# Kernel tuning notes

Hardware: AMD Instinct MI355X
Metric: run time of the kernel (lower is better)

Reference implementation:

```python
import jax, jax.numpy as jnp
import numpy as np

NUM_MODES = 192
LAYERS = [NUM_MODES * 2, 256, 128, 32]


def setup_inputs() -> dict:
    key = jax.random.key(0)
    ks = jax.random.split(key, 7)
    B, C, L = 64, 512, 1024
    x = jax.random.normal(ks[0], (B, C, L), dtype=jnp.float32)
    params = {}
    for i in range(3):
        fan_in, fan_out = LAYERS[i], LAYERS[i + 1]
        bound = 1.0 / np.sqrt(fan_in)
        params[f"W{i+1}"] = jax.random.uniform(ks[1 + 2 * i], (fan_in, fan_out), dtype=jnp.float32, minval=-bound, maxval=bound)
        params[f"b{i+1}"] = jax.random.uniform(ks[2 + 2 * i], (fan_out,), dtype=jnp.float32, minval=-bound, maxval=bound)
    return {"x": x, **params}


def reference(x, W1, b1, W2, b2, W3, b3):
    # rfft over last dim -> complex [B, C, L//2+1]
    f = jnp.fft.rfft(x, axis=-1)
    # view_as_real + slice first NUM_MODES bins -> [B, C, NUM_MODES, 2] (real, imag interleaved)
    f = f[..., :NUM_MODES]
    feat = jnp.stack([f.real, f.imag], axis=-1).reshape(*x.shape[:-1], NUM_MODES * 2)
    h = jax.nn.leaky_relu(feat @ W1 + b1, negative_slope=0.01)
    h = jax.nn.leaky_relu(h @ W2 + b2, negative_slope=0.01)
    return h @ W3 + b3
```

## Files before the change

### kernel.cpp

```cpp
#include <hip/hip_runtime.h>
#include <hip/hip_bf16.h>

typedef __attribute__((ext_vector_type(8))) short short8;
typedef __attribute__((ext_vector_type(4))) float f32x4;

__device__ __forceinline__ short8 load_af(const unsigned short* p) {
  union { uint2 u[2]; short8 v; } r;
  r.u[0] = *(const uint2*)(p);
  r.u[1] = *(const uint2*)(p + 16);
  return r.v;
}

__device__ __forceinline__ unsigned int pk_bf16(float a, float b) {
  __hip_bfloat162 h = __float22bfloat162_rn(make_float2(a, b));
  return *(unsigned int*)&h;
}
__device__ __forceinline__ unsigned short s_bf16(float a) {
  __hip_bfloat16 h = __float2bfloat16(a);
  return *(unsigned short*)&h;
}

__global__ __launch_bounds__(256) void prep_kernel(
    const float* __restrict__ W1, const float* __restrict__ W2,
    const float* __restrict__ W3,
    unsigned short* __restrict__ fL1, unsigned short* __restrict__ fL2,
    unsigned short* __restrict__ fL3) {
  const int w = blockIdx.x * 4 + (threadIdx.x >> 6);
  const int lane = threadIdx.x & 63;
  const int rlo = lane & 15;
  const int q4 = (lane >> 4) << 2;

  if (w < 512) {
    const int nt = w >> 5, kk = w & 31;
    const int col = nt * 16 + rlo;
    const int k0 = kk * 32 + q4;
    float pc[8], ps[8], dc[8], dsn[8], acc[8];
#pragma unroll
    for (int e = 0; e < 8; ++e) {
      int ke = k0 + (e & 3) + ((e >> 2) << 4);
      float ang = (float)ke * 6.135923151542565e-3f;
      float s, c;
      __sincosf(ang, &s, &c);
      dc[e] = c; dsn[e] = s;
      pc[e] = 1.f; ps[e] = 0.f;
      acc[e] = 0.f;
    }
    const float* pw = W1 + col;
#pragma unroll 2
    for (int m = 0; m < 192; ++m) {
      float wre = pw[0];
      float wio = pw[256];
      pw += 512;
#pragma unroll
      for (int e = 0; e < 8; ++e) {
        acc[e] = fmaf(pc[e], wre, acc[e]);
        acc[e] = fmaf(-ps[e], wio, acc[e]);
        float c2 = pc[e] * dc[e] - ps[e] * dsn[e];
        float s2 = ps[e] * dc[e] + pc[e] * dsn[e];
        pc[e] = c2; ps[e] = s2;
      }
    }
    uint4 v;
    v.x = pk_bf16(acc[0], acc[1]);
    v.y = pk_bf16(acc[2], acc[3]);
    v.z = pk_bf16(acc[4], acc[5]);
    v.w = pk_bf16(acc[6], acc[7]);
    *(uint4*)(fL1 + ((size_t)w * 64 + lane) * 8) = v;
  } else if (w < 576) {
    const int tl = w - 512;
    const int nt = tl >> 3, kk = tl & 7;
    const int col = nt * 16 + rlo;
    const int k0 = kk * 32 + q4;
    float a[8];
#pragma unroll
    for (int e = 0; e < 8; ++e) {
      int ke = k0 + (e & 3) + ((e >> 2) << 4);
      a[e] = W2[ke * 128 + col];
    }
    uint4 v;
    v.x = pk_bf16(a[0], a[1]); v.y = pk_bf16(a[2], a[3]);
    v.z = pk_bf16(a[4], a[5]); v.w = pk_bf16(a[6], a[7]);
    *(uint4*)(fL2 + ((size_t)tl * 64 + lane) * 8) = v;
  } else {
    const int tl = w - 576;
    const int nt = tl >> 2, kk = tl & 3;
    const int col = nt * 16 + rlo;
    const int k0 = kk * 32 + q4;
    float a[8];
#pragma unroll
    for (int e = 0; e < 8; ++e) {
      int ke = k0 + (e & 3) + ((e >> 2) << 4);
      a[e] = W3[ke * 32 + col];
    }
    uint4 v;
    v.x = pk_bf16(a[0], a[1]); v.y = pk_bf16(a[2], a[3]);
    v.z = pk_bf16(a[4], a[5]); v.w = pk_bf16(a[6], a[7]);
    *(uint4*)(fL3 + ((size_t)tl * 64 + lane) * 8) = v;
  }
}

#define XS_S 132
#define H1_S 260
#define H2_S 132

struct P2 {
  unsigned short h1[64 * H1_S];
  unsigned short h2[64 * H2_S];
};
union SH {
  unsigned short xs[2][64 * XS_S];
  P2 p2;
};

__global__ __launch_bounds__(256, 3) void mlp_kernel(
    const float* __restrict__ x,
    const float* __restrict__ b1, const float* __restrict__ b2,
    const float* __restrict__ b3,
    const unsigned short* __restrict__ fL1, const unsigned short* __restrict__ fL2,
    const unsigned short* __restrict__ fL3, float* __restrict__ out) {
  __shared__ SH sh;
  const int t = threadIdx.x;
  const int lane = t & 63;
  const int wid = t >> 6;
  const int rlo = lane & 15;
  const int g4 = (lane >> 4) << 2;
  const size_t row0 = (size_t)blockIdx.x * 64;
  const float* xb = x + row0 * 1024;

  f32x4 acc[4][4] = {};

  float4 st[8];
#pragma unroll
  for (int i = 0; i < 8; ++i) {
    int idx = i * 256 + t;
    int row = idx >> 5, cg = idx & 31;
    st[i] = *(const float4*)(xb + row * 1024 + cg * 4);
  }

  for (int kc = 0; kc < 8; ++kc) {
    unsigned short* xbuf = sh.xs[kc & 1];
#pragma unroll
    for (int i = 0; i < 8; ++i) {
      int idx = i * 256 + t;
      int row = idx >> 5, cg = idx & 31;
      uint2 wv;
      wv.x = pk_bf16(st[i].x, st[i].y);
      wv.y = pk_bf16(st[i].z, st[i].w);
      *(uint2*)(xbuf + row * XS_S + cg * 4) = wv;
    }
    if (kc < 7) {
#pragma unroll
      for (int i = 0; i < 8; ++i) {
        int idx = i * 256 + t;
        int row = idx >> 5, cg = idx & 31;
        st[i] = *(const float4*)(xb + row * 1024 + (kc + 1) * 128 + cg * 4);
      }
    }
    short8 bcur[4];
#pragma unroll
    for (int c = 0; c < 4; ++c)
      bcur[c] = *(const short8*)(fL1 +
                (((size_t)(wid * 4 + c) * 32 + kc * 4) * 64 + lane) * 8);
    __syncthreads();
#pragma unroll
    for (int ks = 0; ks < 4; ++ks) {
      short8 bnext[4];
      if (ks < 3) {
#pragma unroll
        for (int c = 0; c < 4; ++c)
          bnext[c] = *(const short8*)(fL1 +
                    (((size_t)(wid * 4 + c) * 32 + kc * 4 + ks + 1) * 64 + lane) * 8);
      }
      short8 af[4];
#pragma unroll
      for (int m = 0; m < 4; ++m)
        af[m] = load_af(xbuf + (m * 16 + rlo) * XS_S + ks * 32 + g4);
#pragma unroll
      for (int m = 0; m < 4; ++m)
#pragma unroll
        for (int c = 0; c < 4; ++c)
          acc[m][c] = __builtin_amdgcn_mfma_f32_16x16x32_bf16(af[m], bcur[c], acc[m][c], 0, 0, 0);
      if (ks < 3) {
#pragma unroll
        for (int c = 0; c < 4; ++c) bcur[c] = bnext[c];
      }
    }
  }
  __syncthreads();

  {
    float bv[4];
#pragma unroll
    for (int c = 0; c < 4; ++c) bv[c] = b1[wid * 64 + c * 16 + rlo];
#pragma unroll
    for (int m = 0; m < 4; ++m)
#pragma unroll
      for (int c = 0; c < 4; ++c)
#pragma unroll
        for (int r = 0; r < 4; ++r) {
          float v = acc[m][c][r] + bv[c];
          v = fmaxf(v, 0.01f * v);
          sh.p2.h1[(m * 16 + g4 + r) * H1_S + wid * 64 + c * 16 + rlo] = s_bf16(v);
        }
  }
  __syncthreads();

  f32x4 a2[4][2] = {};
#pragma unroll
  for (int ks = 0; ks < 8; ++ks) {
    short8 af[4];
#pragma unroll
    for (int m = 0; m < 4; ++m)
      af[m] = load_af(sh.p2.h1 + (m * 16 + rlo) * H1_S + ks * 32 + g4);
    short8 bfr[2];
#pragma unroll
    for (int c = 0; c < 2; ++c)
      bfr[c] = *(const short8*)(fL2 + (((size_t)(wid * 2 + c) * 8 + ks) * 64 + lane) * 8);
#pragma unroll
    for (int m = 0; m < 4; ++m)
#pragma unroll
      for (int c = 0; c < 2; ++c)
        a2[m][c] = __builtin_amdgcn_mfma_f32_16x16x32_bf16(af[m], bfr[c], a2[m][c], 0, 0, 0);
  }
  {
    float bv[2];
#pragma unroll
    for (int c = 0; c < 2; ++c) bv[c] = b2[wid * 32 + c * 16 + rlo];
#pragma unroll
    for (int m = 0; m < 4; ++m)
#pragma unroll
      for (int c = 0; c < 2; ++c)
#pragma unroll
        for (int r = 0; r < 4; ++r) {
          float v = a2[m][c][r] + bv[c];
          v = fmaxf(v, 0.01f * v);
          sh.p2.h2[(m * 16 + g4 + r) * H2_S + wid * 32 + c * 16 + rlo] = s_bf16(v);
        }
  }
  __syncthreads();

  f32x4 a3[2] = {};
#pragma unroll
  for (int ks = 0; ks < 4; ++ks) {
    short8 af = load_af(sh.p2.h2 + (wid * 16 + rlo) * H2_S + ks * 32 + g4);
#pragma unroll
    for (int c = 0; c < 2; ++c) {
      short8 bfr = *(const short8*)(fL3 + (((size_t)c * 4 + ks) * 64 + lane) * 8);
      a3[c] = __builtin_amdgcn_mfma_f32_16x16x32_bf16(af, bfr, a3[c], 0, 0, 0);
    }
  }
  {
    float bv[2];
    bv[0] = b3[rlo];
    bv[1] = b3[16 + rlo];
#pragma unroll
    for (int c = 0; c < 2; ++c)
#pragma unroll
      for (int r = 0; r < 4; ++r)
        out[(row0 + wid * 16 + g4 + r) * 32 + c * 16 + rlo] = a3[c][r] + bv[c];
  }
}

extern "C" void kernel_launch(void* const* d_in, const int* in_sizes, int n_in,
                              void* d_out, int out_size, void* d_ws, size_t ws_size,
                              hipStream_t stream) {
  const float* x  = (const float*)d_in[0];
  const float* W1 = (const float*)d_in[1];
  const float* b1 = (const float*)d_in[2];
  const float* W2 = (const float*)d_in[3];
  const float* b2 = (const float*)d_in[4];
  const float* W3 = (const float*)d_in[5];
  const float* b3 = (const float*)d_in[6];
  float* out = (float*)d_out;

  char* ws = (char*)d_ws;
  unsigned short* fL1 = (unsigned short*)ws;
  unsigned short* fL2 = (unsigned short*)(ws + 524288);
  unsigned short* fL3 = (unsigned short*)(ws + 589824);

  hipLaunchKernelGGL(prep_kernel, dim3(146), dim3(256), 0, stream,
                     W1, W2, W3, fL1, fL2, fL3);
  hipLaunchKernelGGL(mlp_kernel, dim3(512), dim3(256), 0, stream,
                     x, b1, b2, b3, fL1, fL2, fL3, out);
}
```

Baseline: 291.2 us.

## Load x fragments directly from global into registers, drop LDS staging

The first-layer GEMM no longer stages x tiles through a double-buffered LDS buffer. Each wave now loads its own MFMA A-fragments from global memory as float4 pairs, converts them to bf16 in registers, and prefetches one k-step ahead, which removes the LDS writes, reads and per-chunk barriers. The cost is that every one of the 4 waves reads the same x rows redundantly (4x global/L2 traffic for x), the loads are less coalesced, and register pressure rises, so launch bounds drop to 2 blocks per CU.

```diff
diff --git a/kernel.cpp b/kernel.cpp
--- a/kernel.cpp
+++ b/kernel.cpp
@@ -18,6 +18,15 @@
 __device__ __forceinline__ unsigned short s_bf16(float a) {
   __hip_bfloat16 h = __float2bfloat16(a);
   return *(unsigned short*)&h;
+}
+
+__device__ __forceinline__ short8 cvt_af(const float4& lo, const float4& hi) {
+  union { uint4 u; short8 v; } r;
+  r.u.x = pk_bf16(lo.x, lo.y);
+  r.u.y = pk_bf16(lo.z, lo.w);
+  r.u.z = pk_bf16(hi.x, hi.y);
+  r.u.w = pk_bf16(hi.z, hi.w);
+  return r.v;
 }
 
 __global__ __launch_bounds__(256) void prep_kernel(
@@ -99,94 +108,67 @@
   }
 }
 
-#define XS_S 132
 #define H1_S 260
 #define H2_S 132
 
-struct P2 {
-  unsigned short h1[64 * H1_S];
-  unsigned short h2[64 * H2_S];
-};
-union SH {
-  unsigned short xs[2][64 * XS_S];
-  P2 p2;
-};
-
-__global__ __launch_bounds__(256, 3) void mlp_kernel(
+__global__ __launch_bounds__(256, 2) void mlp_kernel(
     const float* __restrict__ x,
     const float* __restrict__ b1, const float* __restrict__ b2,
     const float* __restrict__ b3,
     const unsigned short* __restrict__ fL1, const unsigned short* __restrict__ fL2,
     const unsigned short* __restrict__ fL3, float* __restrict__ out) {
-  __shared__ SH sh;
+  __shared__ unsigned short h1s[64 * H1_S];
+  __shared__ unsigned short h2s[64 * H2_S];
   const int t = threadIdx.x;
   const int lane = t & 63;
   const int wid = t >> 6;
   const int rlo = lane & 15;
   const int g4 = (lane >> 4) << 2;
   const size_t row0 = (size_t)blockIdx.x * 64;
-  const float* xb = x + row0 * 1024;
+
+  const float* xb = x + (row0 + rlo) * 1024 + g4;
+  const unsigned short* fb = fL1 + ((size_t)wid * 4 * 32 * 64 + lane) * 8;
 
   f32x4 acc[4][4] = {};
 
-  float4 st[8];
-#pragma unroll
-  for (int i = 0; i < 8; ++i) {
-    int idx = i * 256 + t;
-    int row = idx >> 5, cg = idx & 31;
-    st[i] = *(const float4*)(xb + row * 1024 + cg * 4);
-  }
-
-  for (int kc = 0; kc < 8; ++kc) {
-    unsigned short* xbuf = sh.xs[kc & 1];
-#pragma unroll
-    for (int i = 0; i < 8; ++i) {
-      int idx = i * 256 + t;
-      int row = idx >> 5, cg = idx & 31;
-      uint2 wv;
-      wv.x = pk_bf16(st[i].x, st[i].y);
-      wv.y = pk_bf16(st[i].z, st[i].w);
-      *(uint2*)(xbuf + row * XS_S + cg * 4) = wv;
-    }
-    if (kc < 7) {
-#pragma unroll
-      for (int i = 0; i < 8; ++i) {
-        int idx = i * 256 + t;
-        int row = idx >> 5, cg = idx & 31;
-        st[i] = *(const float4*)(xb + row * 1024 + (kc + 1) * 128 + cg * 4);
+  float4 ac[4][2], an[4][2];
+  short8 bc[4], bn[4];
+#pragma unroll
+  for (int m = 0; m < 4; ++m) {
+    ac[m][0] = *(const float4*)(xb + m * 16384);
+    ac[m][1] = *(const float4*)(xb + m * 16384 + 16);
+  }
+#pragma unroll
+  for (int c = 0; c < 4; ++c)
+    bc[c] = *(const short8*)(fb + (size_t)c * 32 * 512);
+
+#pragma unroll 2
+  for (int kk = 0; kk < 32; ++kk) {
+    if (kk < 31) {
+#pragma unroll
+      for (int m = 0; m < 4; ++m) {
+        an[m][0] = *(const float4*)(xb + m * 16384 + (kk + 1) * 32);
+        an[m][1] = *(const float4*)(xb + m * 16384 + (kk + 1) * 32 + 16);
       }
-    }
-    short8 bcur[4];
-#pragma unroll
-    for (int c = 0; c < 4; ++c)
-      bcur[c] = *(const short8*)(fL1 +
-                (((size_t)(wid * 4 + c) * 32 + kc * 4) * 64 + lane) * 8);
-    __syncthreads();
-#pragma unroll
-    for (int ks = 0; ks < 4; ++ks) {
-      short8 bnext[4];
-      if (ks < 3) {
-#pragma unroll
-        for (int c = 0; c < 4; ++c)
-          bnext[c] = *(const short8*)(fL1 +
-                    (((size_t)(wid * 4 + c) * 32 + kc * 4 + ks + 1) * 64 + lane) * 8);
-      }
-      short8 af[4];
-#pragma unroll
-      for (int m = 0; m < 4; ++m)
-        af[m] = load_af(xbuf + (m * 16 + rlo) * XS_S + ks * 32 + g4);
-#pragma unroll
-      for (int m = 0; m < 4; ++m)
-#pragma unroll
-        for (int c = 0; c < 4; ++c)
-          acc[m][c] = __builtin_amdgcn_mfma_f32_16x16x32_bf16(af[m], bcur[c], acc[m][c], 0, 0, 0);
-      if (ks < 3) {
-#pragma unroll
-        for (int c = 0; c < 4; ++c) bcur[c] = bnext[c];
-      }
-    }
-  }
-  __syncthreads();
+#pragma unroll
+      for (int c = 0; c < 4; ++c)
+        bn[c] = *(const short8*)(fb + ((size_t)c * 32 + kk + 1) * 512);
+    }
+    short8 af[4];
+#pragma unroll
+    for (int m = 0; m < 4; ++m) af[m] = cvt_af(ac[m][0], ac[m][1]);
+#pragma unroll
+    for (int m = 0; m < 4; ++m)
+#pragma unroll
+      for (int c = 0; c < 4; ++c)
+        acc[m][c] = __builtin_amdgcn_mfma_f32_16x16x32_bf16(af[m], bc[c], acc[m][c], 0, 0, 0);
+    if (kk < 31) {
+#pragma unroll
+      for (int m = 0; m < 4; ++m) { ac[m][0] = an[m][0]; ac[m][1] = an[m][1]; }
+#pragma unroll
+      for (int c = 0; c < 4; ++c) bc[c] = bn[c];
+    }
+  }
 
   {
     float bv[4];
@@ -200,7 +182,7 @@
         for (int r = 0; r < 4; ++r) {
           float v = acc[m][c][r] + bv[c];
           v = fmaxf(v, 0.01f * v);
-          sh.p2.h1[(m * 16 + g4 + r) * H1_S + wid * 64 + c * 16 + rlo] = s_bf16(v);
+          h1s[(m * 16 + g4 + r) * H1_S + wid * 64 + c * 16 + rlo] = s_bf16(v);
         }
   }
   __syncthreads();
@@ -211,7 +193,7 @@
     short8 af[4];
 #pragma unroll
     for (int m = 0; m < 4; ++m)
-      af[m] = load_af(sh.p2.h1 + (m * 16 + rlo) * H1_S + ks * 32 + g4);
+      af[m] = load_af(h1s + (m * 16 + rlo) * H1_S + ks * 32 + g4);
     short8 bfr[2];
 #pragma unroll
     for (int c = 0; c < 2; ++c)
@@ -234,7 +216,7 @@
         for (int r = 0; r < 4; ++r) {
           float v = a2[m][c][r] + bv[c];
           v = fmaxf(v, 0.01f * v);
-          sh.p2.h2[(m * 16 + g4 + r) * H2_S + wid * 32 + c * 16 + rlo] = s_bf16(v);
+          h2s[(m * 16 + g4 + r) * H2_S + wid * 32 + c * 16 + rlo] = s_bf16(v);
         }
   }
   __syncthreads();
@@ -242,7 +224,7 @@
   f32x4 a3[2] = {};
 #pragma unroll
   for (int ks = 0; ks < 4; ++ks) {
-    short8 af = load_af(sh.p2.h2 + (wid * 16 + rlo) * H2_S + ks * 32 + g4);
+    short8 af = load_af(h2s + (wid * 16 + rlo) * H2_S + ks * 32 + g4);
 #pragma unroll
     for (int c = 0; c < 2; ++c) {
       short8 bfr = *(const short8*)(fL3 + (((size_t)c * 4 + ks) * 64 + lane) * 8);
```

New measurement: 291.9 us. Within noise of the previous version (+0.2%).
